# Kernel optimization log

Measured on AMD Instinct MI355X. Metric: run time of the kernel, lower is better.

Reference implementation:

```python
import jax, jax.numpy as jnp
import numpy as np

HEADS = 12
DIM_HEAD = 64
SCALE = DIM_HEAD ** -0.5


def _attn(q, k, v):
    # q: [B, I, D], k/v: [B, J, D]
    sim = jnp.einsum('bid,bjd->bij', q, k)
    a = jax.nn.softmax(sim, axis=-1)
    out = jnp.einsum('bij,bjd->bid', a, v)
    return out, a


def setup_inputs() -> dict:
    key = jax.random.key(0)
    k1, k2, k3 = jax.random.split(key, 3)
    B, F, N, DIM = 8, 8, 196, 768
    x = jax.random.normal(k1, (B, 1 + F * N, DIM), dtype=jnp.float32)
    W_qkv = jax.random.normal(k2, (DIM, 3 * HEADS * DIM_HEAD), dtype=jnp.float32) * (DIM ** -0.5)
    W_out = jax.random.normal(k3, (HEADS * DIM_HEAD, DIM), dtype=jnp.float32) * ((HEADS * DIM_HEAD) ** -0.5)
    b_out = jnp.zeros((DIM,), dtype=jnp.float32)
    return {"x": x, "W_qkv": W_qkv, "W_out": W_out, "b_out": b_out, "f": F}


def reference(x, W_qkv, W_out, b_out, f):
    b, n_tot, dim = x.shape
    h, d = HEADS, DIM_HEAD
    qkv = x @ W_qkv                              # [b, n, 3*h*d]
    q, k, v = jnp.split(qkv, 3, axis=-1)
    # 'b n (h d) -> (b h) n d'
    def to_bh(t):
        return t.reshape(b, n_tot, h, d).transpose(0, 2, 1, 3).reshape(b * h, n_tot, d)
    q, k, v = map(to_bh, (q, k, v))
    q = q * SCALE
    cls_q, q_ = q[:, :1], q[:, 1:]
    cls_k, k_ = k[:, :1], k[:, 1:]
    cls_v, v_ = v[:, :1], v[:, 1:]
    # cls token attends over full sequence
    cls_out, cls_attn = _attn(cls_q, k, v)       # [(b h), 1, d], [(b h), 1, n_tot]
    # spatial attention: 'b (f n) d -> (b f) n d'
    bh = b * h
    n = (n_tot - 1) // f
    def to_bf(t):
        return t.reshape(bh, f, n, d).reshape(bh * f, n, d)
    q_, k_, v_ = map(to_bf, (q_, k_, v_))
    r = f  # q_.shape[0] // cls_k.shape[0]
    # repeat 'b () d -> (b r) () d'
    cls_k_r = jnp.repeat(cls_k, r, axis=0)       # [(bh f), 1, d]
    cls_v_r = jnp.repeat(cls_v, r, axis=0)
    k_ = jnp.concatenate((cls_k_r, k_), axis=1)  # [(bh f), 1+n, d]
    v_ = jnp.concatenate((cls_v_r, v_), axis=1)
    out, _ = _attn(q_, k_, v_)                   # [(bh f), n, d]
    # '(b f) n d -> b (f n) d' (with b := bh)
    out = out.reshape(bh, f * n, d)
    out = jnp.concatenate((cls_out, out), axis=1)  # [(b h), n_tot, d]
    # '(b h) n d -> b n (h d)'
    out = out.reshape(b, h, n_tot, d).transpose(0, 2, 1, 3).reshape(b, n_tot, h * d)
    return out @ W_out + b_out, cls_attn
```

## Files before the change

kernel.cpp:

```cpp
#include <hip/hip_runtime.h>

typedef unsigned short u16;
typedef unsigned int u32;
typedef __attribute__((ext_vector_type(8))) short s16x8;
typedef __attribute__((ext_vector_type(4))) float f32x4;
typedef __attribute__((ext_vector_type(4))) u32 u32x4;
typedef __attribute__((ext_vector_type(4))) float fvec4;

#define DEV static __device__ __forceinline__

typedef __attribute__((address_space(1))) unsigned char ga_u8;
typedef __attribute__((address_space(3))) unsigned char la_u8;

DEV u16 f2bf(float f){
  u32 u = __builtin_bit_cast(u32, f);
  u32 r = (u + 0x7FFFu + ((u >> 16) & 1u)) >> 16;
  return (u16)r;
}
DEV float bf2f(u16 v){
  u32 x = ((u32)v) << 16;
  return __builtin_bit_cast(float, x);
}
DEV f32x4 mfma16(s16x8 a, s16x8 b, f32x4 c){
  return __builtin_amdgcn_mfma_f32_16x16x32_bf16(a, b, c, 0, 0, 0);
}
DEV s16x8 ld16B(const u16* p){
  return __builtin_bit_cast(s16x8, *(const u32x4*)p);
}
DEV u32 cvt_pk_bf16(float lo, float hi){
  u32 r;
  asm volatile("v_cvt_pk_bf16_f32 %0, %1, %2" : "=v"(r) : "v"(lo), "v"(hi));
  return r;
}
DEV void gload16(const void* g, void* l){
  __builtin_amdgcn_global_load_lds((const ga_u8*)g, (la_u8*)l, 16, 0, 0);
}
DEV int xcd_chunk(int bid, int nwg){
  int q = nwg >> 3, r = nwg & 7;
  int xcd = bid & 7, lin = bid >> 3;
  return (xcd < r ? xcd*(q+1) : r*(q+1) + (xcd-r)*q) + lin;
}

#define BARRIER() __builtin_amdgcn_s_barrier()
#define VMC4()    asm volatile("s_waitcnt vmcnt(4)" ::: "memory")
#define VMC0()    asm volatile("s_waitcnt vmcnt(0)" ::: "memory")


__global__ __launch_bounds__(256) void k_prep(const float* __restrict__ x, u16* __restrict__ xb,
                                              const float* __restrict__ Wqkv, u16* __restrict__ wqkvT,
                                              const float* __restrict__ Wout, u16* __restrict__ woutT){
  __shared__ float tile[32][33];
  int b = blockIdx.x, tid = threadIdx.x;
  if (b < 2048){
    const int n4 = 12552*768/4;
    for (int i = b*256 + tid; i < n4; i += 2048*256){
      fvec4 v = ((const fvec4*)x)[i];
      u32 lo = (u32)f2bf(v[0]) | ((u32)f2bf(v[1]) << 16);
      u32 hi = (u32)f2bf(v[2]) | ((u32)f2bf(v[3]) << 16);
      ((u32*)xb)[2*i]   = lo;
      ((u32*)xb)[2*i+1] = hi;
    }
    return;
  }
  const float* W; u16* WT; int K, N, bn, bk;
  if (b < 2048 + 1728){
    int bb = b - 2048; W = Wqkv; WT = wqkvT; K = 768; N = 2304;
    bn = (bb % 72) * 32; bk = (bb / 72) * 32;
  } else {
    int bb = b - 3776; W = Wout; WT = woutT; K = 768; N = 768;
    bn = (bb % 24) * 32; bk = (bb / 24) * 32;
  }
  int tx = tid & 31, ty = tid >> 5;
  #pragma unroll
  for (int r = ty; r < 32; r += 8)
    tile[r][tx] = W[(size_t)(bk + r)*N + bn + tx];
  __syncthreads();
  #pragma unroll
  for (int r = ty; r < 32; r += 8)
    WT[(size_t)(bn + r)*K + bk + tx] = f2bf(tile[tx][r]);
}

__global__ __launch_bounds__(512, 2) void gemm_qkv(const u16* __restrict__ A, const u16* __restrict__ BT,
                                                   u16* __restrict__ qout, u16* __restrict__ kout, u16* __restrict__ vout){
  __shared__ u16 sA[2][2][128*64];
  __shared__ u16 sB[2][2][128*64];
  const int M = 12552;
  const int NWG = 50*9;
  int logical = xcd_chunk(blockIdx.x, NWG);
  int bxi = logical % 9, byi = logical / 9;
  int bm = byi * 256, bn = bxi * 256;

  int tid = threadIdx.x;
  int w = tid >> 6, l = tid & 63, l15 = l & 15, l4 = l >> 4;
  int wm = w >> 2, wn = w & 3;
  int swz = (l15 & 7) << 3;

  f32x4 acc[8][4];
  #pragma unroll
  for (int a=0;a<8;a++)
    #pragma unroll
    for (int b=0;b<4;b++) acc[a][b] = (f32x4){0.f,0.f,0.f,0.f};

  auto stageA = [&](int dbuf, int h, int kt){
    #pragma unroll
    for (int i=0;i<2;i++){
      int ci = i*512 + tid;
      int cs = ci ^ ((ci>>3)&7);
      int r = cs>>3, cc = (cs&7)*8;
      int gr = bm + h*128 + r; if (gr >= M) gr = M-1;
      gload16(A + (size_t)gr*768 + kt*64 + cc, &sA[dbuf][h][(i*512 + (w<<6))*8]);
    }
  };
  auto stageB = [&](int dbuf, int h, int kt){
    #pragma unroll
    for (int i=0;i<2;i++){
      int ci = i*512 + tid;
      int cs = ci ^ ((ci>>3)&7);
      int r = cs>>3, cc = (cs&7)*8;
      gload16(BT + (size_t)(bn + h*128 + r)*768 + kt*64 + cc, &sB[dbuf][h][(i*512 + (w<<6))*8]);
    }
  };

  s16x8 af[4][2], bf[4][2];
  #define LDA_(d, mi, kk) ld16B(&sA[d][wm][(((mi)*16 + l15)*64 + (kk)*32 + l4*8) ^ swz])
  #define LDB_(d, ni, kk) ld16B(&sB[d][(wn*64 + (ni)*16 + l15)>>7][((((wn*64 + (ni)*16 + l15)&127))*64 + (kk)*32 + l4*8) ^ swz])
  #define QUAD(MH, NH) do{ \
    __builtin_amdgcn_s_setprio(1); \
    _Pragma("unroll") \
    for (int j=0;j<4;j++){ \
      _Pragma("unroll") \
      for (int n=0;n<2;n++){ \
        acc[(MH)*4+j][(NH)*2+n] = mfma16(af[j][0], bf[(NH)*2+n][0], acc[(MH)*4+j][(NH)*2+n]); \
        acc[(MH)*4+j][(NH)*2+n] = mfma16(af[j][1], bf[(NH)*2+n][1], acc[(MH)*4+j][(NH)*2+n]); \
      } } \
    __builtin_amdgcn_s_setprio(0); }while(0)

  stageA(0,0,0); stageA(0,1,0); stageB(0,0,0); stageB(0,1,0);
  stageA(1,0,1); stageA(1,1,1);
  VMC4();
  BARRIER();

  #pragma unroll 1
  for (int it = 0; it < 6; ++it){
    int kt1 = 2*it + 1;
    bool full = (it < 5);
    #pragma unroll
    for (int j=0;j<4;j++){ af[j][0]=LDA_(0,j,0); af[j][1]=LDA_(0,j,1); }
    #pragma unroll
    for (int n=0;n<2;n++){ bf[n][0]=LDB_(0,n,0); bf[n][1]=LDB_(0,n,1); }
    stageB(1, 0, kt1);
    BARRIER();
    QUAD(0,0);
    BARRIER();
    #pragma unroll
    for (int n=2;n<4;n++){ bf[n][0]=LDB_(0,n,0); bf[n][1]=LDB_(0,n,1); }
    stageB(1, 1, kt1);
    BARRIER();
    QUAD(0,1);
    BARRIER();
    #pragma unroll
    for (int j=0;j<4;j++){ af[j][0]=LDA_(0,4+j,0); af[j][1]=LDA_(0,4+j,1); }
    if (full){ stageA(0, 0, kt1+1); stageA(0, 1, kt1+1); }
    BARRIER();
    QUAD(1,0); QUAD(1,1);
    if (full) { VMC4(); } else { VMC0(); }
    BARRIER();
    #pragma unroll
    for (int j=0;j<4;j++){ af[j][0]=LDA_(1,j,0); af[j][1]=LDA_(1,j,1); }
    #pragma unroll
    for (int n=0;n<2;n++){ bf[n][0]=LDB_(1,n,0); bf[n][1]=LDB_(1,n,1); }
    if (full) stageB(0, 0, kt1+1);
    BARRIER();
    QUAD(0,0);
    BARRIER();
    #pragma unroll
    for (int n=2;n<4;n++){ bf[n][0]=LDB_(1,n,0); bf[n][1]=LDB_(1,n,1); }
    if (full) stageB(0, 1, kt1+1);
    BARRIER();
    QUAD(0,1);
    BARRIER();
    #pragma unroll
    for (int j=0;j<4;j++){ af[j][0]=LDA_(1,4+j,0); af[j][1]=LDA_(1,4+j,1); }
    if (full){ stageA(1, 0, kt1+2); stageA(1, 1, kt1+2); }
    BARRIER();
    QUAD(1,0); QUAD(1,1);
    if (full) VMC4();
    BARRIER();
  }
  #undef LDA_
  #undef LDB_
  #undef QUAD

  int which = bn / 768;
  int h = ((bn - which*768) >> 6) + wn;
  u16* dst  = (which==0) ? qout : ((which==1) ? kout : vout);
  float scale = (which==0) ? 0.125f : 1.f;
  #pragma unroll
  for (int mi=0; mi<8; mi++){
    #pragma unroll
    for (int r=0; r<4; r++){
      int m = bm + wm*128 + mi*16 + l4*4 + r;
      if (m >= M) continue;
      int b = m / 1569, t = m - b*1569;
      u16* drow = dst + ((size_t)(b*12 + h)*1569 + t)*64 + l15;
      #pragma unroll
      for (int n=0; n<4; n++)
        drow[n*16] = f2bf(acc[mi][n][r] * scale);
    }
  }
}

__global__ __launch_bounds__(256) void cls_a(const u16* __restrict__ qb, const u16* __restrict__ kb,
                                             const u16* __restrict__ vb, float* __restrict__ simw,
                                             float* __restrict__ bsum, float* __restrict__ pvp){
  int c = blockIdx.x, g = blockIdx.y;
  int tid = threadIdx.x;
  __shared__ float qv[64];
  __shared__ float e_lds[256];
  __shared__ float red[256];
  if (tid < 64) qv[tid] = bf2f(qb[(size_t)g*1569*64 + tid]);
  __syncthreads();
  int j = c*256 + tid;
  float e = 0.f;
  if (j < 1569){
    const u16* kr = kb + ((size_t)g*1569 + j)*64;
    float a = 0.f;
    #pragma unroll
    for (int d0 = 0; d0 < 64; d0 += 8){
      u32x4 u = *(const u32x4*)(kr + d0);
      const u16* us = (const u16*)&u;
      #pragma unroll
      for (int i=0;i<8;i++) a += qv[d0+i]*bf2f(us[i]);
    }
    e = __expf(a - 8.f);
    simw[(size_t)g*1569 + j] = e;
  }
  e_lds[tid] = e;
  red[tid] = e; __syncthreads();
  for (int st=128; st>0; st>>=1){ if (tid<st) red[tid] += red[tid+st]; __syncthreads(); }
  if (tid == 0) bsum[g*8 + c] = red[0];
  int d = tid & 63, kk = tid >> 6;
  float a = 0.f;
  for (int jj = kk; jj < 256; jj += 4){
    int jg = c*256 + jj;
    if (jg < 1569) a += e_lds[jj] * bf2f(vb[((size_t)g*1569+jg)*64 + d]);
  }
  red[tid] = a; __syncthreads();
  if (tid < 64) pvp[((size_t)g*7 + c)*64 + tid] = red[tid]+red[tid+64]+red[tid+128]+red[tid+192];
}

__global__ __launch_bounds__(256) void cls_b(const float* __restrict__ simw, const float* __restrict__ bsum,
                                             const float* __restrict__ pvp, float* __restrict__ attn,
                                             u16* __restrict__ ob){
  int g = blockIdx.x, tid = threadIdx.x;
  float s = 0.f;
  #pragma unroll
  for (int c=0;c<7;c++) s += bsum[g*8+c];
  float inv = 1.f/s;
  for (int j = tid; j < 1569; j += 256)
    attn[(size_t)g*1569+j] = simw[(size_t)g*1569+j]*inv;
  if (tid < 64){
    float a = 0.f;
    #pragma unroll
    for (int c=0;c<7;c++) a += pvp[((size_t)g*7+c)*64 + tid];
    ob[(size_t)g*1569*64 + tid] = f2bf(a*inv);
  }
}

__global__ __launch_bounds__(256) void k_frame(const u16* __restrict__ qb, const u16* __restrict__ kb,
                                               const u16* __restrict__ vb, u16* __restrict__ ob){
  int g = blockIdx.x;
  int bh = g >> 3, fi = g & 7;
  int tid = threadIdx.x;
  int w = tid >> 6, l = tid & 63;
  int l15 = l & 15, l4 = l >> 4;

  __shared__ u16 Ks[208][72];
  __shared__ u16 Vt[64][232];
  __shared__ float rs_lds[4][64];

  const u16* qg = qb + ((size_t)bh*1569 + 1 + fi*196)*64;
  const u16* kg = kb + (size_t)bh*1569*64;
  const u16* vg = vb + (size_t)bh*1569*64;

  {
    int jj = tid >> 3, c = (tid & 7)*8;
    #pragma unroll
    for (int base = 0; base < 224; base += 32){
      int j = base + jj;
      u32x4 kv = {0,0,0,0}, vv = {0,0,0,0};
      if (j < 197){
        int t = (j == 0) ? 0 : (1 + fi*196 + j - 1);
        kv = *(const u32x4*)(kg + (size_t)t*64 + c);
        vv = *(const u32x4*)(vg + (size_t)t*64 + c);
      }
      if (j < 208) *(u32x4*)&Ks[j][c] = kv;
      int jl = j & 31;
      int col = (j & ~31) + ((jl>>2)&3)*8 + (jl>>4)*4 + (jl&3);
      const u16* vp = (const u16*)&vv;
      #pragma unroll
      for (int i=0;i<8;i++) Vt[c+i][col] = vp[i];
    }
  }

  s16x8 qf[4][2];
  #pragma unroll
  for (int mt=0; mt<4; mt++){
    int row = w*64 + mt*16 + l15;
    #pragma unroll
    for (int kk=0; kk<2; kk++){
      if (row < 196) qf[mt][kk] = ld16B(qg + (size_t)row*64 + kk*32 + l4*8);
      else { u32x4 z = {0,0,0,0}; qf[mt][kk] = __builtin_bit_cast(s16x8, z); }
    }
  }

  f32x4 acc[4][4];
  float rsum[4] = {0.f, 0.f, 0.f, 0.f};
  #pragma unroll
  for (int a=0;a<4;a++)
    #pragma unroll
    for (int b=0;b<4;b++) acc[a][b] = (f32x4){0.f,0.f,0.f,0.f};

  __syncthreads();

  for (int ck = 0; ck < 7; ck++){
    int r0 = ck*32 + l15;
    int r1 = r0 + 16; if (r1 > 207) r1 = 207;
    s16x8 kf0[2], kf1[2];
    #pragma unroll
    for (int kk=0; kk<2; kk++){
      kf0[kk] = ld16B(&Ks[r0][kk*32 + l4*8]);
      kf1[kk] = ld16B(&Ks[r1][kk*32 + l4*8]);
    }
    s16x8 vf[4];
    #pragma unroll
    for (int ntd=0; ntd<4; ntd++) vf[ntd] = ld16B(&Vt[ntd*16 + l15][ck*32 + l4*8]);
    int kbase = ck*32 + l4*4;

    #pragma unroll
    for (int mt=0; mt<4; mt++){
      __builtin_amdgcn_s_setprio(1);
      f32x4 s0 = (f32x4){0.f,0.f,0.f,0.f}, s1 = (f32x4){0.f,0.f,0.f,0.f};
      s0 = mfma16(kf0[0], qf[mt][0], s0);
      s0 = mfma16(kf0[1], qf[mt][1], s0);
      s1 = mfma16(kf1[0], qf[mt][0], s1);
      s1 = mfma16(kf1[1], qf[mt][1], s1);
      __builtin_amdgcn_s_setprio(0);
      float p[8];
      #pragma unroll
      for (int r=0; r<4; r++){
        p[r]   = (kbase + r      < 197) ? __expf(s0[r] - 8.f) : 0.f;
        p[4+r] = (kbase + 16 + r < 197) ? __expf(s1[r] - 8.f) : 0.f;
      }
      rsum[mt] += ((p[0]+p[1])+(p[2]+p[3])) + ((p[4]+p[5])+(p[6]+p[7]));
      u32x4 pw;
      pw[0] = cvt_pk_bf16(p[0], p[1]);
      pw[1] = cvt_pk_bf16(p[2], p[3]);
      pw[2] = cvt_pk_bf16(p[4], p[5]);
      pw[3] = cvt_pk_bf16(p[6], p[7]);
      s16x8 pa = __builtin_bit_cast(s16x8, pw);
      __builtin_amdgcn_s_setprio(1);
      #pragma unroll
      for (int ntd=0; ntd<4; ntd++)
        acc[mt][ntd] = mfma16(pa, vf[ntd], acc[mt][ntd]);
      __builtin_amdgcn_s_setprio(0);
    }
  }

  #pragma unroll
  for (int mt=0; mt<4; mt++){
    float rs = rsum[mt];
    rs += __shfl_xor(rs, 16);
    rs += __shfl_xor(rs, 32);
    rs_lds[w][mt*16 + l15] = rs;
  }

  u16* og = ob + ((size_t)bh*1569 + 1 + fi*196)*64;
  #pragma unroll
  for (int mt=0; mt<4; mt++){
    #pragma unroll
    for (int r=0; r<4; r++){
      int row = w*64 + mt*16 + l4*4 + r;
      if (row < 196){
        float inv = 1.f / rs_lds[w][mt*16 + l4*4 + r];
        #pragma unroll
        for (int ntd=0; ntd<4; ntd++)
          og[(size_t)row*64 + ntd*16 + l15] = f2bf(acc[mt][ntd][r] * inv);
      }
    }
  }
}

__global__ __launch_bounds__(512, 2) void gemm_out(const u16* __restrict__ AO, const u16* __restrict__ BT,
                                                   const float* __restrict__ bias, float* __restrict__ C){
  __shared__ u16 sA[2][2][128*64];
  __shared__ u16 sB[2][2][128*64];
  const int M = 12552;
  const int NWG = 50*3;
  int logical = xcd_chunk(blockIdx.x, NWG);
  int bxi = logical % 3, byi = logical / 3;
  int bm = byi * 256, bn = bxi * 256;

  int tid = threadIdx.x;
  int w = tid >> 6, l = tid & 63, l15 = l & 15, l4 = l >> 4;
  int wm = w >> 2, wn = w & 3;
  int swz = (l15 & 7) << 3;

  f32x4 acc[8][4];
  #pragma unroll
  for (int a=0;a<8;a++)
    #pragma unroll
    for (int b=0;b<4;b++) acc[a][b] = (f32x4){0.f,0.f,0.f,0.f};

  auto stageA = [&](int dbuf, int h, int kt){
    #pragma unroll
    for (int i=0;i<2;i++){
      int ci = i*512 + tid;
      int cs = ci ^ ((ci>>3)&7);
      int r = cs>>3, cc = (cs&7)*8;
      int gr = bm + h*128 + r; if (gr >= M) gr = M-1;
      int b = gr / 1569, t = gr - b*1569;
      gload16(AO + ((size_t)(b*12 + kt)*1569 + t)*64 + cc, &sA[dbuf][h][(i*512 + (w<<6))*8]);
    }
  };
  auto stageB = [&](int dbuf, int h, int kt){
    #pragma unroll
    for (int i=0;i<2;i++){
      int ci = i*512 + tid;
      int cs = ci ^ ((ci>>3)&7);
      int r = cs>>3, cc = (cs&7)*8;
      gload16(BT + (size_t)(bn + h*128 + r)*768 + kt*64 + cc, &sB[dbuf][h][(i*512 + (w<<6))*8]);
    }
  };

  s16x8 af[4][2], bf[4][2];
  #define LDA_(d, mi, kk) ld16B(&sA[d][wm][(((mi)*16 + l15)*64 + (kk)*32 + l4*8) ^ swz])
  #define LDB_(d, ni, kk) ld16B(&sB[d][(wn*64 + (ni)*16 + l15)>>7][((((wn*64 + (ni)*16 + l15)&127))*64 + (kk)*32 + l4*8) ^ swz])
  #define QUAD(MH, NH) do{ \
    __builtin_amdgcn_s_setprio(1); \
    _Pragma("unroll") \
    for (int j=0;j<4;j++){ \
      _Pragma("unroll") \
      for (int n=0;n<2;n++){ \
        acc[(MH)*4+j][(NH)*2+n] = mfma16(af[j][0], bf[(NH)*2+n][0], acc[(MH)*4+j][(NH)*2+n]); \
        acc[(MH)*4+j][(NH)*2+n] = mfma16(af[j][1], bf[(NH)*2+n][1], acc[(MH)*4+j][(NH)*2+n]); \
      } } \
    __builtin_amdgcn_s_setprio(0); }while(0)

  stageA(0,0,0); stageA(0,1,0); stageB(0,0,0); stageB(0,1,0);
  stageA(1,0,1); stageA(1,1,1);
  VMC4();
  BARRIER();

  #pragma unroll 1
  for (int it = 0; it < 6; ++it){
    int kt1 = 2*it + 1;
    bool full = (it < 5);
    #pragma unroll
    for (int j=0;j<4;j++){ af[j][0]=LDA_(0,j,0); af[j][1]=LDA_(0,j,1); }
    #pragma unroll
    for (int n=0;n<2;n++){ bf[n][0]=LDB_(0,n,0); bf[n][1]=LDB_(0,n,1); }
    stageB(1, 0, kt1);
    BARRIER();
    QUAD(0,0);
    BARRIER();
    #pragma unroll
    for (int n=2;n<4;n++){ bf[n][0]=LDB_(0,n,0); bf[n][1]=LDB_(0,n,1); }
    stageB(1, 1, kt1);
    BARRIER();
    QUAD(0,1);
    BARRIER();
    #pragma unroll
    for (int j=0;j<4;j++){ af[j][0]=LDA_(0,4+j,0); af[j][1]=LDA_(0,4+j,1); }
    if (full){ stageA(0, 0, kt1+1); stageA(0, 1, kt1+1); }
    BARRIER();
    QUAD(1,0); QUAD(1,1);
    if (full) { VMC4(); } else { VMC0(); }
    BARRIER();
    #pragma unroll
    for (int j=0;j<4;j++){ af[j][0]=LDA_(1,j,0); af[j][1]=LDA_(1,j,1); }
    #pragma unroll
    for (int n=0;n<2;n++){ bf[n][0]=LDB_(1,n,0); bf[n][1]=LDB_(1,n,1); }
    if (full) stageB(0, 0, kt1+1);
    BARRIER();
    QUAD(0,0);
    BARRIER();
    #pragma unroll
    for (int n=2;n<4;n++){ bf[n][0]=LDB_(1,n,0); bf[n][1]=LDB_(1,n,1); }
    if (full) stageB(0, 1, kt1+1);
    BARRIER();
    QUAD(0,1);
    BARRIER();
    #pragma unroll
    for (int j=0;j<4;j++){ af[j][0]=LDA_(1,4+j,0); af[j][1]=LDA_(1,4+j,1); }
    if (full){ stageA(1, 0, kt1+2); stageA(1, 1, kt1+2); }
    BARRIER();
    QUAD(1,0); QUAD(1,1);
    if (full) VMC4();
    BARRIER();
  }
  #undef LDA_
  #undef LDB_
  #undef QUAD

  int n0 = bn + wn*64;
  float bv[4];
  #pragma unroll
  for (int n=0;n<4;n++) bv[n] = bias[n0 + n*16 + l15];
  #pragma unroll
  for (int mi=0; mi<8; mi++){
    #pragma unroll
    for (int r=0; r<4; r++){
      int m = bm + wm*128 + mi*16 + l4*4 + r;
      if (m >= M) continue;
      float* crow = C + (size_t)m*768 + n0 + l15;
      #pragma unroll
      for (int n=0; n<4; n++)
        crow[n*16] = acc[mi][n][r] + bv[n];
    }
  }
}

extern "C" void kernel_launch(void* const* d_in, const int* in_sizes, int n_in,
                              void* d_out, int out_size, void* d_ws, size_t ws_size,
                              hipStream_t stream){
  (void)in_sizes; (void)n_in; (void)out_size;
  const float* x    = (const float*)d_in[0];
  const float* Wqkv = (const float*)d_in[1];
  const float* Wout = (const float*)d_in[2];
  const float* bout = (const float*)d_in[3];
  float* out0 = (float*)d_out;
  float* out1 = out0 + (size_t)12552*768;

  char* ws = (char*)d_ws;
  size_t off = 0;
  auto alloc = [&](size_t bytes)->char*{
    char* p = ws + off;
    off += (bytes + 255) & ~(size_t)255;
    return p;
  };
  u16* xb    = (u16*)alloc((size_t)12552*768*2);
  u16* wqkvT = (u16*)alloc((size_t)2304*768*2);
  u16* woutT = (u16*)alloc((size_t)768*768*2);
  u16* qb    = (u16*)alloc((size_t)96*1569*64*2);
  u16* kbuf  = (u16*)alloc((size_t)96*1569*64*2);
  u16* vbuf  = (u16*)alloc((size_t)96*1569*64*2);
  u16* ao    = (u16*)alloc((size_t)96*1569*64*2);
  float* simw = (float*)alloc((size_t)96*1569*4);
  float* bsum = (float*)alloc((size_t)96*8*4);
  float* pvp  = (float*)alloc((size_t)96*7*64*4);
  if (off > ws_size) return;

  k_prep<<<4352, 256, 0, stream>>>(x, xb, Wqkv, wqkvT, Wout, woutT);
  gemm_qkv<<<50*9, 512, 0, stream>>>(xb, wqkvT, qb, kbuf, vbuf);
  cls_a<<<dim3(7, 96), 256, 0, stream>>>(qb, kbuf, vbuf, simw, bsum, pvp);
  cls_b<<<96, 256, 0, stream>>>(simw, bsum, pvp, out1, ao);
  k_frame<<<768, 256, 0, stream>>>(qb, kbuf, vbuf, ao);
  gemm_out<<<50*3, 512, 0, stream>>>(ao, woutT, bout, out0);
}
```

Before: 172.0 us.

## Use 32x32 MFMA tiles in both GEMMs and merge cls/frame attention kernels

Both GEMMs now use the 32x32x16 bf16 MFMA, with f32x16 accumulators and fragment loads and epilogue indexing adjusted to match. This issues fewer MFMA instructions and fewer LDS fragment reads per tile. Separately, the cls_a and k_frame kernels are merged into one k_attn launch whose extra blocks run the cls partial work, which removes a launch and lets the two workloads run concurrently. The risks are different register pressure, possible LDS bank conflicts with the new swizzle, and LDS being sized for the larger branch in every block.

New measurement: 186.2 us. 8.3% more time.

```diff
diff --git a/kernel.cpp b/kernel.cpp
--- a/kernel.cpp
+++ b/kernel.cpp
@@ -4,6 +4,7 @@
 typedef unsigned int u32;
 typedef __attribute__((ext_vector_type(8))) short s16x8;
 typedef __attribute__((ext_vector_type(4))) float f32x4;
+typedef __attribute__((ext_vector_type(16))) float f32x16;
 typedef __attribute__((ext_vector_type(4))) u32 u32x4;
 typedef __attribute__((ext_vector_type(4))) float fvec4;
 
@@ -23,6 +24,9 @@
 }
 DEV f32x4 mfma16(s16x8 a, s16x8 b, f32x4 c){
   return __builtin_amdgcn_mfma_f32_16x16x32_bf16(a, b, c, 0, 0, 0);
+}
+DEV f32x16 mfma32(s16x8 a, s16x8 b, f32x16 c){
+  return __builtin_amdgcn_mfma_f32_32x32x16_bf16(a, b, c, 0, 0, 0);
 }
 DEV s16x8 ld16B(const u16* p){
   return __builtin_bit_cast(s16x8, *(const u32x4*)p);
@@ -91,15 +95,18 @@
   int bm = byi * 256, bn = bxi * 256;
 
   int tid = threadIdx.x;
-  int w = tid >> 6, l = tid & 63, l15 = l & 15, l4 = l >> 4;
+  int w = tid >> 6, l = tid & 63;
+  int l31 = l & 31, lhi = l >> 5;
   int wm = w >> 2, wn = w & 3;
-  int swz = (l15 & 7) << 3;
-
-  f32x4 acc[8][4];
-  #pragma unroll
-  for (int a=0;a<8;a++)
-    #pragma unroll
-    for (int b=0;b<4;b++) acc[a][b] = (f32x4){0.f,0.f,0.f,0.f};
+  int swz = (l & 7) << 3;
+
+  f32x16 acc[4][2];
+  #pragma unroll
+  for (int a=0;a<4;a++)
+    #pragma unroll
+    for (int b=0;b<2;b++)
+      #pragma unroll
+      for (int e=0;e<16;e++) acc[a][b][e] = 0.f;
 
   auto stageA = [&](int dbuf, int h, int kt){
     #pragma unroll
@@ -121,18 +128,17 @@
     }
   };
 
-  s16x8 af[4][2], bf[4][2];
-  #define LDA_(d, mi, kk) ld16B(&sA[d][wm][(((mi)*16 + l15)*64 + (kk)*32 + l4*8) ^ swz])
-  #define LDB_(d, ni, kk) ld16B(&sB[d][(wn*64 + (ni)*16 + l15)>>7][((((wn*64 + (ni)*16 + l15)&127))*64 + (kk)*32 + l4*8) ^ swz])
+  s16x8 af[2][4], bf[2][4];
+  #define LDA_(d, mt, ks) ld16B(&sA[d][wm][(((mt)*32 + l31)*64 + (ks)*16 + lhi*8) ^ swz])
+  #define LDB_(d, nt, ks) ld16B(&sB[d][(wn*64 + (nt)*32 + l31)>>7][(((wn*64 + (nt)*32 + l31)&127)*64 + (ks)*16 + lhi*8) ^ swz])
   #define QUAD(MH, NH) do{ \
     __builtin_amdgcn_s_setprio(1); \
     _Pragma("unroll") \
-    for (int j=0;j<4;j++){ \
+    for (int m2=0;m2<2;m2++){ \
       _Pragma("unroll") \
-      for (int n=0;n<2;n++){ \
-        acc[(MH)*4+j][(NH)*2+n] = mfma16(af[j][0], bf[(NH)*2+n][0], acc[(MH)*4+j][(NH)*2+n]); \
-        acc[(MH)*4+j][(NH)*2+n] = mfma16(af[j][1], bf[(NH)*2+n][1], acc[(MH)*4+j][(NH)*2+n]); \
-      } } \
+      for (int ks=0;ks<4;ks++) \
+        acc[(MH)*2+m2][NH] = mfma32(af[m2][ks], bf[NH][ks], acc[(MH)*2+m2][NH]); \
+    } \
     __builtin_amdgcn_s_setprio(0); }while(0)
 
   stageA(0,0,0); stageA(0,1,0); stageB(0,0,0); stageB(0,1,0);
@@ -145,42 +151,50 @@
     int kt1 = 2*it + 1;
     bool full = (it < 5);
     #pragma unroll
-    for (int j=0;j<4;j++){ af[j][0]=LDA_(0,j,0); af[j][1]=LDA_(0,j,1); }
-    #pragma unroll
-    for (int n=0;n<2;n++){ bf[n][0]=LDB_(0,n,0); bf[n][1]=LDB_(0,n,1); }
+    for (int m2=0;m2<2;m2++)
+      #pragma unroll
+      for (int ks=0;ks<4;ks++) af[m2][ks]=LDA_(0,m2,ks);
+    #pragma unroll
+    for (int ks=0;ks<4;ks++) bf[0][ks]=LDB_(0,0,ks);
     stageB(1, 0, kt1);
     BARRIER();
     QUAD(0,0);
     BARRIER();
     #pragma unroll
-    for (int n=2;n<4;n++){ bf[n][0]=LDB_(0,n,0); bf[n][1]=LDB_(0,n,1); }
+    for (int ks=0;ks<4;ks++) bf[1][ks]=LDB_(0,1,ks);
     stageB(1, 1, kt1);
     BARRIER();
     QUAD(0,1);
     BARRIER();
     #pragma unroll
-    for (int j=0;j<4;j++){ af[j][0]=LDA_(0,4+j,0); af[j][1]=LDA_(0,4+j,1); }
+    for (int m2=0;m2<2;m2++)
+      #pragma unroll
+      for (int ks=0;ks<4;ks++) af[m2][ks]=LDA_(0,2+m2,ks);
     if (full){ stageA(0, 0, kt1+1); stageA(0, 1, kt1+1); }
     BARRIER();
     QUAD(1,0); QUAD(1,1);
     if (full) { VMC4(); } else { VMC0(); }
     BARRIER();
     #pragma unroll
-    for (int j=0;j<4;j++){ af[j][0]=LDA_(1,j,0); af[j][1]=LDA_(1,j,1); }
-    #pragma unroll
-    for (int n=0;n<2;n++){ bf[n][0]=LDB_(1,n,0); bf[n][1]=LDB_(1,n,1); }
+    for (int m2=0;m2<2;m2++)
+      #pragma unroll
+      for (int ks=0;ks<4;ks++) af[m2][ks]=LDA_(1,m2,ks);
+    #pragma unroll
+    for (int ks=0;ks<4;ks++) bf[0][ks]=LDB_(1,0,ks);
     if (full) stageB(0, 0, kt1+1);
     BARRIER();
     QUAD(0,0);
     BARRIER();
     #pragma unroll
-    for (int n=2;n<4;n++){ bf[n][0]=LDB_(1,n,0); bf[n][1]=LDB_(1,n,1); }
+    for (int ks=0;ks<4;ks++) bf[1][ks]=LDB_(1,1,ks);
     if (full) stageB(0, 1, kt1+1);
     BARRIER();
     QUAD(0,1);
     BARRIER();
     #pragma unroll
-    for (int j=0;j<4;j++){ af[j][0]=LDA_(1,4+j,0); af[j][1]=LDA_(1,4+j,1); }
+    for (int m2=0;m2<2;m2++)
+      #pragma unroll
+      for (int ks=0;ks<4;ks++) af[m2][ks]=LDA_(1,2+m2,ks);
     if (full){ stageA(1, 0, kt1+2); stageA(1, 1, kt1+2); }
     BARRIER();
     QUAD(1,0); QUAD(1,1);
@@ -196,88 +210,72 @@
   u16* dst  = (which==0) ? qout : ((which==1) ? kout : vout);
   float scale = (which==0) ? 0.125f : 1.f;
   #pragma unroll
-  for (int mi=0; mi<8; mi++){
-    #pragma unroll
-    for (int r=0; r<4; r++){
-      int m = bm + wm*128 + mi*16 + l4*4 + r;
+  for (int mt=0; mt<4; mt++){
+    #pragma unroll
+    for (int reg=0; reg<16; reg++){
+      int m = bm + wm*128 + mt*32 + (reg&3) + ((reg>>2)<<3) + (lhi<<2);
       if (m >= M) continue;
       int b = m / 1569, t = m - b*1569;
-      u16* drow = dst + ((size_t)(b*12 + h)*1569 + t)*64 + l15;
-      #pragma unroll
-      for (int n=0; n<4; n++)
-        drow[n*16] = f2bf(acc[mi][n][r] * scale);
-    }
-  }
-}
-
-__global__ __launch_bounds__(256) void cls_a(const u16* __restrict__ qb, const u16* __restrict__ kb,
-                                             const u16* __restrict__ vb, float* __restrict__ simw,
-                                             float* __restrict__ bsum, float* __restrict__ pvp){
-  int c = blockIdx.x, g = blockIdx.y;
-  int tid = threadIdx.x;
-  __shared__ float qv[64];
-  __shared__ float e_lds[256];
-  __shared__ float red[256];
-  if (tid < 64) qv[tid] = bf2f(qb[(size_t)g*1569*64 + tid]);
-  __syncthreads();
-  int j = c*256 + tid;
-  float e = 0.f;
-  if (j < 1569){
-    const u16* kr = kb + ((size_t)g*1569 + j)*64;
-    float a = 0.f;
-    #pragma unroll
-    for (int d0 = 0; d0 < 64; d0 += 8){
-      u32x4 u = *(const u32x4*)(kr + d0);
-      const u16* us = (const u16*)&u;
-      #pragma unroll
-      for (int i=0;i<8;i++) a += qv[d0+i]*bf2f(us[i]);
-    }
-    e = __expf(a - 8.f);
-    simw[(size_t)g*1569 + j] = e;
-  }
-  e_lds[tid] = e;
-  red[tid] = e; __syncthreads();
-  for (int st=128; st>0; st>>=1){ if (tid<st) red[tid] += red[tid+st]; __syncthreads(); }
-  if (tid == 0) bsum[g*8 + c] = red[0];
-  int d = tid & 63, kk = tid >> 6;
-  float a = 0.f;
-  for (int jj = kk; jj < 256; jj += 4){
-    int jg = c*256 + jj;
-    if (jg < 1569) a += e_lds[jj] * bf2f(vb[((size_t)g*1569+jg)*64 + d]);
-  }
-  red[tid] = a; __syncthreads();
-  if (tid < 64) pvp[((size_t)g*7 + c)*64 + tid] = red[tid]+red[tid+64]+red[tid+128]+red[tid+192];
-}
-
-__global__ __launch_bounds__(256) void cls_b(const float* __restrict__ simw, const float* __restrict__ bsum,
-                                             const float* __restrict__ pvp, float* __restrict__ attn,
-                                             u16* __restrict__ ob){
-  int g = blockIdx.x, tid = threadIdx.x;
-  float s = 0.f;
-  #pragma unroll
-  for (int c=0;c<7;c++) s += bsum[g*8+c];
-  float inv = 1.f/s;
-  for (int j = tid; j < 1569; j += 256)
-    attn[(size_t)g*1569+j] = simw[(size_t)g*1569+j]*inv;
-  if (tid < 64){
-    float a = 0.f;
-    #pragma unroll
-    for (int c=0;c<7;c++) a += pvp[((size_t)g*7+c)*64 + tid];
-    ob[(size_t)g*1569*64 + tid] = f2bf(a*inv);
-  }
-}
-
-__global__ __launch_bounds__(256) void k_frame(const u16* __restrict__ qb, const u16* __restrict__ kb,
-                                               const u16* __restrict__ vb, u16* __restrict__ ob){
-  int g = blockIdx.x;
-  int bh = g >> 3, fi = g & 7;
-  int tid = threadIdx.x;
-  int w = tid >> 6, l = tid & 63;
-  int l15 = l & 15, l4 = l >> 4;
-
+      u16* drow = dst + ((size_t)(b*12 + h)*1569 + t)*64;
+      #pragma unroll
+      for (int nt=0; nt<2; nt++)
+        drow[nt*32 + l31] = f2bf(acc[mt][nt][reg] * scale);
+    }
+  }
+}
+
+__global__ __launch_bounds__(256) void k_attn(const u16* __restrict__ qb, const u16* __restrict__ kb,
+                                              const u16* __restrict__ vb, u16* __restrict__ ob,
+                                              float* __restrict__ simw, float* __restrict__ bsum,
+                                              float* __restrict__ pvp){
   __shared__ u16 Ks[208][72];
   __shared__ u16 Vt[64][232];
   __shared__ float rs_lds[4][64];
+
+  int blk = blockIdx.x, tid = threadIdx.x;
+
+  if (blk >= 768){
+    int bb = blk - 768;
+    int c = bb % 7, g = bb / 7;
+    __shared__ float qv[64];
+    __shared__ float e_lds[256];
+    __shared__ float red[256];
+    if (tid < 64) qv[tid] = bf2f(qb[(size_t)g*1569*64 + tid]);
+    __syncthreads();
+    int j = c*256 + tid;
+    float e = 0.f;
+    if (j < 1569){
+      const u16* kr = kb + ((size_t)g*1569 + j)*64;
+      float a = 0.f;
+      #pragma unroll
+      for (int d0 = 0; d0 < 64; d0 += 8){
+        u32x4 u = *(const u32x4*)(kr + d0);
+        const u16* us = (const u16*)&u;
+        #pragma unroll
+        for (int i=0;i<8;i++) a += qv[d0+i]*bf2f(us[i]);
+      }
+      e = __expf(a - 8.f);
+      simw[(size_t)g*1569 + j] = e;
+    }
+    e_lds[tid] = e;
+    red[tid] = e; __syncthreads();
+    for (int st=128; st>0; st>>=1){ if (tid<st) red[tid] += red[tid+st]; __syncthreads(); }
+    if (tid == 0) bsum[g*8 + c] = red[0];
+    int d = tid & 63, kk = tid >> 6;
+    float a = 0.f;
+    for (int jj = kk; jj < 256; jj += 4){
+      int jg = c*256 + jj;
+      if (jg < 1569) a += e_lds[jj] * bf2f(vb[((size_t)g*1569+jg)*64 + d]);
+    }
+    red[tid] = a; __syncthreads();
+    if (tid < 64) pvp[((size_t)g*7 + c)*64 + tid] = red[tid]+red[tid+64]+red[tid+128]+red[tid+192];
+    return;
+  }
+
+  int g = blk;
+  int bh = g >> 3, fi = g & 7;
+  int w = tid >> 6, l = tid & 63;
+  int l15 = l & 15, l4 = l >> 4;
 
   const u16* qg = qb + ((size_t)bh*1569 + 1 + fi*196)*64;
   const u16* kg = kb + (size_t)bh*1569*64;
@@ -391,6 +389,24 @@
   }
 }
 
+__global__ __launch_bounds__(256) void cls_b(const float* __restrict__ simw, const float* __restrict__ bsum,
+                                             const float* __restrict__ pvp, float* __restrict__ attn,
+                                             u16* __restrict__ ob){
+  int g = blockIdx.x, tid = threadIdx.x;
+  float s = 0.f;
+  #pragma unroll
+  for (int c=0;c<7;c++) s += bsum[g*8+c];
+  float inv = 1.f/s;
+  for (int j = tid; j < 1569; j += 256)
+    attn[(size_t)g*1569+j] = simw[(size_t)g*1569+j]*inv;
+  if (tid < 64){
+    float a = 0.f;
+    #pragma unroll
+    for (int c=0;c<7;c++) a += pvp[((size_t)g*7+c)*64 + tid];
+    ob[(size_t)g*1569*64 + tid] = f2bf(a*inv);
+  }
+}
+
 __global__ __launch_bounds__(512, 2) void gemm_out(const u16* __restrict__ AO, const u16* __restrict__ BT,
                                                    const float* __restrict__ bias, float* __restrict__ C){
   __shared__ u16 sA[2][2][128*64];
@@ -402,15 +418,18 @@
   int bm = byi * 256, bn = bxi * 256;
 
   int tid = threadIdx.x;
-  int w = tid >> 6, l = tid & 63, l15 = l & 15, l4 = l >> 4;
+  int w = tid >> 6, l = tid & 63;
+  int l31 = l & 31, lhi = l >> 5;
   int wm = w >> 2, wn = w & 3;
-  int swz = (l15 & 7) << 3;
-
-  f32x4 acc[8][4];
-  #pragma unroll
-  for (int a=0;a<8;a++)
-    #pragma unroll
-    for (int b=0;b<4;b++) acc[a][b] = (f32x4){0.f,0.f,0.f,0.f};
+  int swz = (l & 7) << 3;
+
+  f32x16 acc[4][2];
+  #pragma unroll
+  for (int a=0;a<4;a++)
+    #pragma unroll
+    for (int b=0;b<2;b++)
+      #pragma unroll
+      for (int e=0;e<16;e++) acc[a][b][e] = 0.f;
 
   auto stageA = [&](int dbuf, int h, int kt){
     #pragma unroll
@@ -433,18 +452,17 @@
     }
   };
 
-  s16x8 af[4][2], bf[4][2];
-  #define LDA_(d, mi, kk) ld16B(&sA[d][wm][(((mi)*16 + l15)*64 + (kk)*32 + l4*8) ^ swz])
-  #define LDB_(d, ni, kk) ld16B(&sB[d][(wn*64 + (ni)*16 + l15)>>7][((((wn*64 + (ni)*16 + l15)&127))*64 + (kk)*32 + l4*8) ^ swz])
+  s16x8 af[2][4], bf[2][4];
+  #define LDA_(d, mt, ks) ld16B(&sA[d][wm][(((mt)*32 + l31)*64 + (ks)*16 + lhi*8) ^ swz])
+  #define LDB_(d, nt, ks) ld16B(&sB[d][(wn*64 + (nt)*32 + l31)>>7][(((wn*64 + (nt)*32 + l31)&127)*64 + (ks)*16 + lhi*8) ^ swz])
   #define QUAD(MH, NH) do{ \
     __builtin_amdgcn_s_setprio(1); \
     _Pragma("unroll") \
-    for (int j=0;j<4;j++){ \
+    for (int m2=0;m2<2;m2++){ \
       _Pragma("unroll") \
-      for (int n=0;n<2;n++){ \
-        acc[(MH)*4+j][(NH)*2+n] = mfma16(af[j][0], bf[(NH)*2+n][0], acc[(MH)*4+j][(NH)*2+n]); \
-        acc[(MH)*4+j][(NH)*2+n] = mfma16(af[j][1], bf[(NH)*2+n][1], acc[(MH)*4+j][(NH)*2+n]); \
-      } } \
+      for (int ks=0;ks<4;ks++) \
+        acc[(MH)*2+m2][NH] = mfma32(af[m2][ks], bf[NH][ks], acc[(MH)*2+m2][NH]); \
+    } \
     __builtin_amdgcn_s_setprio(0); }while(0)
 
   stageA(0,0,0); stageA(0,1,0); stageB(0,0,0); stageB(0,1,0);
@@ -457,42 +475,50 @@
     int kt1 = 2*it + 1;
     bool full = (it < 5);
     #pragma unroll
-    for (int j=0;j<4;j++){ af[j][0]=LDA_(0,j,0); af[j][1]=LDA_(0,j,1); }
-    #pragma unroll
-    for (int n=0;n<2;n++){ bf[n][0]=LDB_(0,n,0); bf[n][1]=LDB_(0,n,1); }
+    for (int m2=0;m2<2;m2++)
+      #pragma unroll
+      for (int ks=0;ks<4;ks++) af[m2][ks]=LDA_(0,m2,ks);
+    #pragma unroll
+    for (int ks=0;ks<4;ks++) bf[0][ks]=LDB_(0,0,ks);
     stageB(1, 0, kt1);
     BARRIER();
     QUAD(0,0);
     BARRIER();
     #pragma unroll
-    for (int n=2;n<4;n++){ bf[n][0]=LDB_(0,n,0); bf[n][1]=LDB_(0,n,1); }
+    for (int ks=0;ks<4;ks++) bf[1][ks]=LDB_(0,1,ks);
     stageB(1, 1, kt1);
     BARRIER();
     QUAD(0,1);
     BARRIER();
     #pragma unroll
-    for (int j=0;j<4;j++){ af[j][0]=LDA_(0,4+j,0); af[j][1]=LDA_(0,4+j,1); }
+    for (int m2=0;m2<2;m2++)
+      #pragma unroll
+      for (int ks=0;ks<4;ks++) af[m2][ks]=LDA_(0,2+m2,ks);
     if (full){ stageA(0, 0, kt1+1); stageA(0, 1, kt1+1); }
     BARRIER();
     QUAD(1,0); QUAD(1,1);
     if (full) { VMC4(); } else { VMC0(); }
     BARRIER();
     #pragma unroll
-    for (int j=0;j<4;j++){ af[j][0]=LDA_(1,j,0); af[j][1]=LDA_(1,j,1); }
-    #pragma unroll
-    for (int n=0;n<2;n++){ bf[n][0]=LDB_(1,n,0); bf[n][1]=LDB_(1,n,1); }
+    for (int m2=0;m2<2;m2++)
+      #pragma unroll
+      for (int ks=0;ks<4;ks++) af[m2][ks]=LDA_(1,m2,ks);
+    #pragma unroll
+    for (int ks=0;ks<4;ks++) bf[0][ks]=LDB_(1,0,ks);
     if (full) stageB(0, 0, kt1+1);
     BARRIER();
     QUAD(0,0);
     BARRIER();
     #pragma unroll
-    for (int n=2;n<4;n++){ bf[n][0]=LDB_(1,n,0); bf[n][1]=LDB_(1,n,1); }
+    for (int ks=0;ks<4;ks++) bf[1][ks]=LDB_(1,1,ks);
     if (full) stageB(0, 1, kt1+1);
     BARRIER();
     QUAD(0,1);
     BARRIER();
     #pragma unroll
-    for (int j=0;j<4;j++){ af[j][0]=LDA_(1,4+j,0); af[j][1]=LDA_(1,4+j,1); }
+    for (int m2=0;m2<2;m2++)
+      #pragma unroll
+      for (int ks=0;ks<4;ks++) af[m2][ks]=LDA_(1,2+m2,ks);
     if (full){ stageA(1, 0, kt1+2); stageA(1, 1, kt1+2); }
     BARRIER();
     QUAD(1,0); QUAD(1,1);
@@ -504,19 +530,19 @@
   #undef QUAD
 
   int n0 = bn + wn*64;
-  float bv[4];
-  #pragma unroll
-  for (int n=0;n<4;n++) bv[n] = bias[n0 + n*16 + l15];
-  #pragma unroll
-  for (int mi=0; mi<8; mi++){
-    #pragma unroll
-    for (int r=0; r<4; r++){
-      int m = bm + wm*128 + mi*16 + l4*4 + r;
+  float bv[2];
+  #pragma unroll
+  for (int nt=0;nt<2;nt++) bv[nt] = bias[n0 + nt*32 + l31];
+  #pragma unroll
+  for (int mt=0; mt<4; mt++){
+    #pragma unroll
+    for (int reg=0; reg<16; reg++){
+      int m = bm + wm*128 + mt*32 + (reg&3) + ((reg>>2)<<3) + (lhi<<2);
       if (m >= M) continue;
-      float* crow = C + (size_t)m*768 + n0 + l15;
-      #pragma unroll
-      for (int n=0; n<4; n++)
-        crow[n*16] = acc[mi][n][r] + bv[n];
+      float* crow = C + (size_t)m*768 + n0;
+      #pragma unroll
+      for (int nt=0; nt<2; nt++)
+        crow[nt*32 + l31] = acc[mt][nt][reg] + bv[nt];
     }
   }
 }
@@ -553,8 +579,7 @@
 
   k_prep<<<4352, 256, 0, stream>>>(x, xb, Wqkv, wqkvT, Wout, woutT);
   gemm_qkv<<<50*9, 512, 0, stream>>>(xb, wqkvT, qb, kbuf, vbuf);
-  cls_a<<<dim3(7, 96), 256, 0, stream>>>(qb, kbuf, vbuf, simw, bsum, pvp);
+  k_attn<<<1440, 256, 0, stream>>>(qb, kbuf, vbuf, ao, simw, bsum, pvp);
   cls_b<<<96, 256, 0, stream>>>(simw, bsum, pvp, out1, ao);
-  k_frame<<<768, 256, 0, stream>>>(qb, kbuf, vbuf, ao);
   gemm_out<<<50*3, 512, 0, stream>>>(ao, woutT, bout, out0);
 }
```
